# Kernel tuning notes

Measured on AMD Instinct MI355X. Metric: run time of the kernel, lower is better.

The kernel has to match this reference:

```python
import jax, jax.numpy as jnp
import numpy as np

N_IN = 200000   # active input voxels
N_OUT = 200000  # stride-1 submanifold conv: out_nnz == in_nnz
K_VOL = 27      # 3x3x3 kernel volume
M = 100000      # gathered pairs per kernel offset
C_IN = 64
C_OUT = 64


def setup_inputs() -> dict:
    key = jax.random.key(0)
    k1, k2, k3, k4, k5 = jax.random.split(key, 5)
    in_feats = jax.random.normal(k1, (N_IN, C_IN), dtype=jnp.float32)
    kernel = jax.random.normal(k2, (K_VOL, C_IN, C_OUT), dtype=jnp.float32) * (1.0 / np.sqrt(C_IN))
    bias = jax.random.normal(k3, (C_OUT,), dtype=jnp.float32)
    imap = jax.random.randint(k4, (K_VOL, M), 0, N_IN, dtype=jnp.int32)
    omap = jax.random.randint(k5, (K_VOL, M), 0, N_OUT, dtype=jnp.int32)
    return {"in_feats": in_feats, "kernel": kernel, "bias": bias,
            "imap": imap, "omap": omap}


def reference(in_feats, kernel, bias, imap, omap):
    # Sparse 3D conv: per-kernel-offset gather -> GEMM -> scatter-add.
    # gathered: [K_VOL, M, C_IN]
    gathered = in_feats[imap]
    # per-offset GEMM: [K_VOL, M, C_OUT]
    contrib = jnp.einsum('kmc,kco->kmo', gathered, kernel)
    # scatter-add into output rows: [N_OUT, C_OUT]
    out = jnp.zeros((N_OUT, C_OUT), dtype=in_feats.dtype)
    out = out.at[omap].add(contrib)
    return out + bias
```

## Files before the change

### kernel.cpp

```cpp
#include <hip/hip_runtime.h>
#include <hip/hip_bf16.h>

#define N_IN 200000
#define N_OUT 200000
#define K_VOL 27
#define M_PAIRS 100000
#define C_IN 64
#define C_OUT 64

#define MTILE 64
#define LDS_PAD 72

typedef __attribute__((ext_vector_type(4))) float floatx4;
typedef __attribute__((ext_vector_type(8))) short shortx8;

static __device__ __forceinline__ ushort f32_to_bf16(float f) {
    union { float f; unsigned int u; } x; x.f = f;
    unsigned int u = x.u;
    u += 0x7FFFu + ((u >> 16) & 1u);
    return (ushort)(u >> 16);
}

__global__ void cvt_feats_kernel(const float* __restrict__ src, ushort* __restrict__ dst, int n4) {
    int i = blockIdx.x * blockDim.x + threadIdx.x;
    if (i >= n4) return;
    float4 v = ((const float4*)src)[i];
    ushort4 o;
    o.x = f32_to_bf16(v.x); o.y = f32_to_bf16(v.y);
    o.z = f32_to_bf16(v.z); o.w = f32_to_bf16(v.w);
    ((ushort4*)dst)[i] = o;
}

__global__ void cvt_wt_kernel(const float* __restrict__ w, ushort* __restrict__ wt) {
    int idx = blockIdx.x * blockDim.x + threadIdx.x;
    if (idx >= K_VOL * C_IN * C_OUT) return;
    int k   = idx >> 12;
    int rem = idx & 4095;
    int c   = rem >> 6;
    int o   = rem & 63;
    wt[(k << 12) + (o << 6) + c] = f32_to_bf16(w[idx]);
}

__global__ void init_bias_kernel(const float* __restrict__ bias, float* __restrict__ out, int n4) {
    int i = blockIdx.x * blockDim.x + threadIdx.x;
    if (i >= n4) return;
    int c = (i * 4) & 63;
    float4 b = *(const float4*)(bias + c);
    ((float4*)out)[i] = b;
}

__launch_bounds__(256, 4)
__global__ void spconv_kernel(const ushort* __restrict__ feats,
                              const ushort* __restrict__ wt,
                              const int* __restrict__ imap,
                              const int* __restrict__ omap,
                              float* __restrict__ out) {
    __shared__ ushort Asm[MTILE * LDS_PAD];
    __shared__ ushort Wsm[C_OUT * LDS_PAD];
    __shared__ int omap_s[MTILE];

    const int k   = blockIdx.y;
    const int m0  = blockIdx.x * MTILE;
    const int tid = threadIdx.x;
    const int kM  = k * M_PAIRS;

    #pragma unroll
    for (int p = 0; p < 2; ++p) {
        int cid = tid + p * 256;
        int row = cid >> 3;
        int ch  = cid & 7;
        *(shortx8*)&Wsm[row * LDS_PAD + ch * 8] =
            *(const shortx8*)&wt[(k << 12) + row * 64 + ch * 8];
    }
    #pragma unroll
    for (int p = 0; p < 2; ++p) {
        int cid = tid + p * 256;
        int row = cid >> 3;
        int ch  = cid & 7;
        int m   = m0 + row;
        shortx8 v = {0, 0, 0, 0, 0, 0, 0, 0};
        if (m < M_PAIRS) {
            int g = imap[kM + m];
            v = *(const shortx8*)&feats[(g << 6) + ch * 8];
        }
        *(shortx8*)&Asm[row * LDS_PAD + ch * 8] = v;
    }
    if (tid < MTILE) {
        int m = m0 + tid;
        omap_s[tid] = (m < M_PAIRS) ? omap[kM + m] : -1;
    }
    __syncthreads();

    const int wave = tid >> 6;
    const int lane = tid & 63;
    const int quad = lane >> 4;
    const int l16  = lane & 15;
    const int rbase = wave * 16;

    const shortx8 a0 = *(const shortx8*)&Asm[(rbase + l16) * LDS_PAD + quad * 8];
    const shortx8 a1 = *(const shortx8*)&Asm[(rbase + l16) * LDS_PAD + 32 + quad * 8];

    #pragma unroll
    for (int ct = 0; ct < 4; ++ct) {
        const shortx8 b0 = *(const shortx8*)&Wsm[(ct * 16 + l16) * LDS_PAD + quad * 8];
        const shortx8 b1 = *(const shortx8*)&Wsm[(ct * 16 + l16) * LDS_PAD + 32 + quad * 8];
        floatx4 acc = {0.f, 0.f, 0.f, 0.f};
        acc = __builtin_amdgcn_mfma_f32_16x16x32_bf16(a0, b0, acc, 0, 0, 0);
        acc = __builtin_amdgcn_mfma_f32_16x16x32_bf16(a1, b1, acc, 0, 0, 0);

        const int col = ct * 16 + l16;
        #pragma unroll
        for (int r = 0; r < 4; ++r) {
            int rl = rbase + quad * 4 + r;
            int orow = omap_s[rl];
            if (orow >= 0) atomicAdd(&out[(orow << 6) + col], acc[r]);
        }
    }
}

extern "C" void kernel_launch(void* const* d_in, const int* in_sizes, int n_in,
                              void* d_out, int out_size, void* d_ws, size_t ws_size,
                              hipStream_t stream) {
    const float* in_feats = (const float*)d_in[0];
    const float* kernelw  = (const float*)d_in[1];
    const float* bias     = (const float*)d_in[2];
    const int*   imap     = (const int*)d_in[3];
    const int*   omap     = (const int*)d_in[4];
    float* out = (float*)d_out;

    ushort* feats_bf = (ushort*)d_ws;
    ushort* wt_bf    = (ushort*)((char*)d_ws + (size_t)N_IN * C_IN * 2);

    int n4 = N_IN * C_IN / 4;
    cvt_feats_kernel<<<(n4 + 255) / 256, 256, 0, stream>>>(in_feats, feats_bf, n4);
    cvt_wt_kernel<<<(K_VOL * C_IN * C_OUT + 255) / 256, 256, 0, stream>>>(kernelw, wt_bf);
    int o4 = N_OUT * C_OUT / 4;
    init_bias_kernel<<<(o4 + 255) / 256, 256, 0, stream>>>(bias, out, o4);

    dim3 grid((M_PAIRS + MTILE - 1) / MTILE, K_VOL);
    spconv_kernel<<<grid, 256, 0, stream>>>(feats_bf, wt_bf, imap, omap, out);
}
```

Before: 659.1 us.

## Bucket pairs by output row range and accumulate in LDS instead of global atomics

Builds a per-offset, per-output-range bucketing of the (imap, omap) pairs using a count, single-block scan and scatter pipeline. The main conv kernel then gets one block per 128-row output range, accumulates every offset's contributions into LDS with shared-memory atomics, and writes each output row once with the bias added. This removes the 5.4M scattered global float atomics and the separate bias-init pass. In exchange it adds three preprocessing kernels, including a serial one-block scan over about 42k buckets, runs the main kernel as roughly 1.5k blocks, and lets per-block work become uneven.

```diff
diff --git a/kernel.cpp b/kernel.cpp
--- a/kernel.cpp
+++ b/kernel.cpp
@@ -8,8 +8,15 @@
 #define C_IN 64
 #define C_OUT 64
 
+#define RROWS 128
+#define RSHIFT 7
+#define NRANGE ((N_OUT + RROWS - 1) / RROWS)
+#define NBUCKET (K_VOL * NRANGE)
+#define NREC (K_VOL * M_PAIRS)
+
 #define MTILE 64
 #define LDS_PAD 72
+#define ACC_PAD 68
 
 typedef __attribute__((ext_vector_type(4))) float floatx4;
 typedef __attribute__((ext_vector_type(8))) short shortx8;
@@ -41,79 +48,147 @@
     wt[(k << 12) + (o << 6) + c] = f32_to_bf16(w[idx]);
 }
 
-__global__ void init_bias_kernel(const float* __restrict__ bias, float* __restrict__ out, int n4) {
-    int i = blockIdx.x * blockDim.x + threadIdx.x;
-    if (i >= n4) return;
-    int c = (i * 4) & 63;
-    float4 b = *(const float4*)(bias + c);
-    ((float4*)out)[i] = b;
-}
-
-__launch_bounds__(256, 4)
+__global__ void count_kernel(const int* __restrict__ omap, unsigned int* __restrict__ counts) {
+    int m = blockIdx.x * blockDim.x + threadIdx.x;
+    if (m >= M_PAIRS) return;
+    int k = blockIdx.y;
+    int o = omap[k * M_PAIRS + m];
+    atomicAdd(&counts[k * NRANGE + (o >> RSHIFT)], 1u);
+}
+
+__global__ void scan_kernel(const unsigned int* __restrict__ counts,
+                            unsigned int* __restrict__ offsets,
+                            unsigned int* __restrict__ cursor) {
+    __shared__ unsigned int part[256];
+    const int tid = threadIdx.x;
+    const int CH = (NBUCKET + 255) / 256;
+    const int b0 = tid * CH;
+    unsigned int s = 0;
+    for (int j = 0; j < CH; ++j) {
+        int b = b0 + j;
+        if (b < NBUCKET) s += counts[b];
+    }
+    part[tid] = s;
+    __syncthreads();
+    for (int d = 1; d < 256; d <<= 1) {
+        unsigned int v = (tid >= d) ? part[tid - d] : 0u;
+        __syncthreads();
+        part[tid] += v;
+        __syncthreads();
+    }
+    unsigned int run = (tid > 0) ? part[tid - 1] : 0u;
+    for (int j = 0; j < CH; ++j) {
+        int b = b0 + j;
+        if (b < NBUCKET) {
+            offsets[b] = run;
+            cursor[b]  = run;
+            run += counts[b];
+        }
+    }
+    if (tid == 255) offsets[NBUCKET] = run;
+}
+
+__global__ void scatter_kernel(const int* __restrict__ imap, const int* __restrict__ omap,
+                               unsigned int* __restrict__ cursor, unsigned int* __restrict__ records) {
+    int m = blockIdx.x * blockDim.x + threadIdx.x;
+    if (m >= M_PAIRS) return;
+    int k = blockIdx.y;
+    int o = omap[k * M_PAIRS + m];
+    unsigned int g = (unsigned int)imap[k * M_PAIRS + m];
+    unsigned int b = (unsigned int)(k * NRANGE) + (unsigned int)(o >> RSHIFT);
+    unsigned int pos = atomicAdd(&cursor[b], 1u);
+    atomicExch(&records[pos], g | ((unsigned int)(o & (RROWS - 1)) << 18));
+}
+
+__launch_bounds__(256, 3)
 __global__ void spconv_kernel(const ushort* __restrict__ feats,
                               const ushort* __restrict__ wt,
-                              const int* __restrict__ imap,
-                              const int* __restrict__ omap,
+                              const unsigned int* __restrict__ offsets,
+                              const unsigned int* __restrict__ records,
+                              const float* __restrict__ bias,
                               float* __restrict__ out) {
-    __shared__ ushort Asm[MTILE * LDS_PAD];
-    __shared__ ushort Wsm[C_OUT * LDS_PAD];
+    __shared__ __align__(16) float  accs[RROWS * ACC_PAD];
+    __shared__ __align__(16) ushort Asm[MTILE * LDS_PAD];
     __shared__ int omap_s[MTILE];
 
-    const int k   = blockIdx.y;
-    const int m0  = blockIdx.x * MTILE;
     const int tid = threadIdx.x;
-    const int kM  = k * M_PAIRS;
-
+    const int bx  = blockIdx.x;
+    const int r0  = bx * RROWS;
+
+    for (int idx = tid; idx < (RROWS * ACC_PAD) / 4; idx += 256)
+        ((float4*)accs)[idx] = make_float4(0.f, 0.f, 0.f, 0.f);
+
+    const int wave  = tid >> 6;
+    const int lane  = tid & 63;
+    const int quad  = lane >> 4;
+    const int l16   = lane & 15;
+    const int rbase = wave * 16;
+
+    for (int k = 0; k < K_VOL; ++k) {
+        const unsigned int beg = offsets[k * NRANGE + bx];
+        const unsigned int end = offsets[k * NRANGE + bx + 1];
+        if (beg == end) continue;
+
+        shortx8 bf0[4], bf1[4];
+        #pragma unroll
+        for (int ct = 0; ct < 4; ++ct) {
+            const ushort* wp = &wt[(k << 12) + (ct * 16 + l16) * 64 + quad * 8];
+            bf0[ct] = *(const shortx8*)wp;
+            bf1[ct] = *(const shortx8*)(wp + 32);
+        }
+
+        for (unsigned int t = beg; t < end; t += MTILE) {
+            const unsigned int nrem = end - t;
+            const int n = (nrem > (unsigned int)MTILE) ? MTILE : (int)nrem;
+
+            #pragma unroll
+            for (int p = 0; p < 2; ++p) {
+                int cid = tid + p * 256;
+                int row = cid >> 3;
+                int ch  = cid & 7;
+                shortx8 v = {0, 0, 0, 0, 0, 0, 0, 0};
+                if (row < n) {
+                    unsigned int g = records[t + row] & 0x3FFFFu;
+                    v = *(const shortx8*)&feats[(g << 6) + ch * 8];
+                }
+                *(shortx8*)&Asm[row * LDS_PAD + ch * 8] = v;
+            }
+            if (tid < MTILE)
+                omap_s[tid] = (tid < n) ? (int)((records[t + tid] >> 18) & (RROWS - 1)) : -1;
+            __syncthreads();
+
+            const shortx8 a0 = *(const shortx8*)&Asm[(rbase + l16) * LDS_PAD + quad * 8];
+            const shortx8 a1 = *(const shortx8*)&Asm[(rbase + l16) * LDS_PAD + 32 + quad * 8];
+
+            #pragma unroll
+            for (int ct = 0; ct < 4; ++ct) {
+                floatx4 acc = {0.f, 0.f, 0.f, 0.f};
+                acc = __builtin_amdgcn_mfma_f32_16x16x32_bf16(a0, bf0[ct], acc, 0, 0, 0);
+                acc = __builtin_amdgcn_mfma_f32_16x16x32_bf16(a1, bf1[ct], acc, 0, 0, 0);
+                const int col = ct * 16 + l16;
+                #pragma unroll
+                for (int r = 0; r < 4; ++r) {
+                    int rl = rbase + quad * 4 + r;
+                    int ol = omap_s[rl];
+                    if (ol >= 0) atomicAdd(&accs[ol * ACC_PAD + col], acc[r]);
+                }
+            }
+            __syncthreads();
+        }
+    }
+
+    __syncthreads();
     #pragma unroll
-    for (int p = 0; p < 2; ++p) {
-        int cid = tid + p * 256;
-        int row = cid >> 3;
-        int ch  = cid & 7;
-        *(shortx8*)&Wsm[row * LDS_PAD + ch * 8] =
-            *(const shortx8*)&wt[(k << 12) + row * 64 + ch * 8];
-    }
-    #pragma unroll
-    for (int p = 0; p < 2; ++p) {
-        int cid = tid + p * 256;
-        int row = cid >> 3;
-        int ch  = cid & 7;
-        int m   = m0 + row;
-        shortx8 v = {0, 0, 0, 0, 0, 0, 0, 0};
-        if (m < M_PAIRS) {
-            int g = imap[kM + m];
-            v = *(const shortx8*)&feats[(g << 6) + ch * 8];
-        }
-        *(shortx8*)&Asm[row * LDS_PAD + ch * 8] = v;
-    }
-    if (tid < MTILE) {
-        int m = m0 + tid;
-        omap_s[tid] = (m < M_PAIRS) ? omap[kM + m] : -1;
-    }
-    __syncthreads();
-
-    const int wave = tid >> 6;
-    const int lane = tid & 63;
-    const int quad = lane >> 4;
-    const int l16  = lane & 15;
-    const int rbase = wave * 16;
-
-    const shortx8 a0 = *(const shortx8*)&Asm[(rbase + l16) * LDS_PAD + quad * 8];
-    const shortx8 a1 = *(const shortx8*)&Asm[(rbase + l16) * LDS_PAD + 32 + quad * 8];
-
-    #pragma unroll
-    for (int ct = 0; ct < 4; ++ct) {
-        const shortx8 b0 = *(const shortx8*)&Wsm[(ct * 16 + l16) * LDS_PAD + quad * 8];
-        const shortx8 b1 = *(const shortx8*)&Wsm[(ct * 16 + l16) * LDS_PAD + 32 + quad * 8];
-        floatx4 acc = {0.f, 0.f, 0.f, 0.f};
-        acc = __builtin_amdgcn_mfma_f32_16x16x32_bf16(a0, b0, acc, 0, 0, 0);
-        acc = __builtin_amdgcn_mfma_f32_16x16x32_bf16(a1, b1, acc, 0, 0, 0);
-
-        const int col = ct * 16 + l16;
-        #pragma unroll
-        for (int r = 0; r < 4; ++r) {
-            int rl = rbase + quad * 4 + r;
-            int orow = omap_s[rl];
-            if (orow >= 0) atomicAdd(&out[(orow << 6) + col], acc[r]);
+    for (int i = 0; i < 8; ++i) {
+        int idx  = tid + i * 256;
+        int row  = idx >> 4;
+        int c4   = idx & 15;
+        int orow = r0 + row;
+        if (orow < N_OUT) {
+            float4 v = *(float4*)&accs[row * ACC_PAD + c4 * 4];
+            const float4 bb = *(const float4*)&bias[c4 * 4];
+            v.x += bb.x; v.y += bb.y; v.z += bb.z; v.w += bb.w;
+            *(float4*)&out[(orow << 6) + c4 * 4] = v;
         }
     }
 }
@@ -128,15 +203,24 @@
     const int*   omap     = (const int*)d_in[4];
     float* out = (float*)d_out;
 
-    ushort* feats_bf = (ushort*)d_ws;
-    ushort* wt_bf    = (ushort*)((char*)d_ws + (size_t)N_IN * C_IN * 2);
+    char* p = (char*)d_ws;
+    ushort* feats_bf = (ushort*)p;  p += (size_t)N_IN * C_IN * 2;
+    ushort* wt_bf    = (ushort*)p;  p += (size_t)K_VOL * C_IN * C_OUT * 2;
+    unsigned int* counts  = (unsigned int*)p;  p += (size_t)(NBUCKET + 1) * 4;
+    unsigned int* offsets = (unsigned int*)p;  p += (size_t)(NBUCKET + 1) * 4;
+    unsigned int* cursor  = (unsigned int*)p;  p += (size_t)(NBUCKET + 1) * 4;
+    unsigned int* records = (unsigned int*)p;  p += (size_t)NREC * 4;
+
+    hipMemsetAsync(counts, 0, (size_t)NBUCKET * 4, stream);
 
     int n4 = N_IN * C_IN / 4;
     cvt_feats_kernel<<<(n4 + 255) / 256, 256, 0, stream>>>(in_feats, feats_bf, n4);
     cvt_wt_kernel<<<(K_VOL * C_IN * C_OUT + 255) / 256, 256, 0, stream>>>(kernelw, wt_bf);
-    int o4 = N_OUT * C_OUT / 4;
-    init_bias_kernel<<<(o4 + 255) / 256, 256, 0, stream>>>(bias, out, o4);
-
-    dim3 grid((M_PAIRS + MTILE - 1) / MTILE, K_VOL);
-    spconv_kernel<<<grid, 256, 0, stream>>>(feats_bf, wt_bf, imap, omap, out);
-}
+
+    dim3 gmap((M_PAIRS + 255) / 256, K_VOL);
+    count_kernel<<<gmap, 256, 0, stream>>>(omap, counts);
+    scan_kernel<<<1, 256, 0, stream>>>(counts, offsets, cursor);
+    scatter_kernel<<<gmap, 256, 0, stream>>>(imap, omap, cursor, records);
+
+    spconv_kernel<<<NRANGE, 256, 0, stream>>>(feats_bf, wt_bf, offsets, records, bias, out);
+}
```

Result: slower. 1.686 ms (+155.8%).
